# Performance work log

Hardware: AMD Instinct MI355X
Metric: run time of the kernel (lower is better)

The kernel has to match this reference:

```python
import jax, jax.numpy as jnp
import numpy as np

N_HEAD = 16
N_EMBD = 1024

def setup_inputs() -> dict:
    key = jax.random.key(0)
    ks = jax.random.split(key, 7)
    B, S, D = 2, 2048, N_EMBD
    scale = 1.0 / np.sqrt(D)
    return {
        "x": jax.random.normal(ks[0], (B, S, D), dtype=jnp.float32),
        "Wq": jax.random.normal(ks[1], (D, D), dtype=jnp.float32) * scale,
        "bq": jnp.zeros((D,), dtype=jnp.float32),
        "Wk": jax.random.normal(ks[2], (D, D), dtype=jnp.float32) * scale,
        "bk": jnp.zeros((D,), dtype=jnp.float32),
        "Wv": jax.random.normal(ks[3], (D, D), dtype=jnp.float32) * scale,
        "bv": jnp.zeros((D,), dtype=jnp.float32),
    }

def reference(x, Wq, bq, Wk, bk, Wv, bv):
    B, S, D = x.shape
    H = N_HEAD
    hd = D // H
    # QKV projections
    q = (x @ Wq + bq).reshape(B, S, H, hd).transpose(0, 2, 1, 3)  # [B,H,S,hd]
    k = (x @ Wk + bk).reshape(B, S, H, hd).transpose(0, 2, 1, 3)
    v = (x @ Wv + bv).reshape(B, S, H, hd).transpose(0, 2, 1, 3)
    # Note: original module defines a causal mask but never applies it.
    att = jnp.einsum("bhqd,bhkd->bhqk", q, k) * (1.0 / jnp.sqrt(hd).astype(x.dtype))
    att = jax.nn.softmax(att, axis=-1)
    y = jnp.einsum("bhqk,bhkd->bhqd", att, v)  # [B,H,S,hd]
    return y.transpose(0, 2, 1, 3).reshape(B, S, D)
```

## Files before the change

### kernel.cpp

```cpp
#include <hip/hip_runtime.h>


#define D_MODEL 1024
#define NHEAD   16
#define HDIM    64
#define SEQ     2048
#define MROWS   4096
#define CSC     0.18033688011112042f

typedef __attribute__((ext_vector_type(8))) short short8;
typedef __attribute__((ext_vector_type(4))) float f32x4;

__device__ __forceinline__ float bf2f(unsigned short u) {
  return __uint_as_float(((unsigned int)u) << 16);
}
__device__ __forceinline__ unsigned short f2bf(float f) {
  unsigned int u = __float_as_uint(f);
  u += 0x7fff + ((u >> 16) & 1);
  return (unsigned short)(u >> 16);
}
__device__ __forceinline__ unsigned int cvtpk_bf16(float lo, float hi) {
  unsigned int r;
  asm("v_cvt_pk_bf16_f32 %0, %1, %2" : "=v"(r) : "v"(lo), "v"(hi));
  return r;
}

__device__ __forceinline__ int sniff_bf16(const unsigned short* x) {
  int cnt = 0;
#pragma unroll
  for (int i = 0; i < 64; ++i) {
    const unsigned e = (x[2 * i] >> 7) & 0xFF;
    cnt += (e >= 105 && e <= 140) ? 1 : 0;
  }
  return cnt >= 48;
}

__device__ __forceinline__ void gl_lds16(const unsigned short* g, unsigned short* l) {
  __builtin_amdgcn_global_load_lds(
      (const __attribute__((address_space(1))) unsigned int*)g,
      (__attribute__((address_space(3))) unsigned int*)l, 16, 0, 0);
}

__global__ __launch_bounds__(256) void cvt_x(const unsigned short* __restrict__ X,
                                             unsigned short* __restrict__ Xbf) {
  const int isbf = sniff_bf16(X);
  const size_t i0 = ((size_t)blockIdx.x * 256 + threadIdx.x) * 8;
  if (isbf) {
    *(uint4*)(Xbf + i0) = *(const uint4*)(X + i0);
  } else {
    const float* Xf = (const float*)X;
    const float4 f0 = *(const float4*)(Xf + i0);
    const float4 f1 = *(const float4*)(Xf + i0 + 4);
    unsigned int t[4] = {cvtpk_bf16(f0.x, f0.y), cvtpk_bf16(f0.z, f0.w),
                         cvtpk_bf16(f1.x, f1.y), cvtpk_bf16(f1.z, f1.w)};
    *(uint4*)(Xbf + i0) = *(const uint4*)t;
  }
}

__global__ __launch_bounds__(256) void cvt_w(
    const unsigned short* __restrict__ w0, const unsigned short* __restrict__ w1,
    const unsigned short* __restrict__ w2,
    const unsigned short* __restrict__ b0, const unsigned short* __restrict__ b1,
    const unsigned short* __restrict__ b2,
    unsigned short* __restrict__ Wt, unsigned short* __restrict__ bb) {
  __shared__ unsigned short tile[32][33];
  const int z = blockIdx.z;
  const unsigned short* W    = (z == 0) ? w0 : ((z == 1) ? w1 : w2);
  const unsigned short* bias = (z == 0) ? b0 : ((z == 1) ? b1 : b2);
  unsigned short* Wtz = Wt + ((size_t)z << 20);
  const int isbf = sniff_bf16(W);
  const int bx = blockIdx.x * 32;
  const int by = blockIdx.y * 32;
  const int tx = threadIdx.x & 31;
  const int ty = threadIdx.x >> 5;
#pragma unroll
  for (int r = ty; r < 32; r += 8) {
    unsigned short v;
    if (isbf) v = W[(size_t)(by + r) * D_MODEL + bx + tx];
    else      v = f2bf(((const float*)W)[(size_t)(by + r) * D_MODEL + bx + tx]);
    tile[r][tx] = v;
  }
  __syncthreads();
#pragma unroll
  for (int r = ty; r < 32; r += 8)
    Wtz[(size_t)(bx + r) * D_MODEL + by + tx] = tile[tx][r];
  if (blockIdx.x == 0 && blockIdx.y == 0) {
    const int i0 = threadIdx.x * 4;
#pragma unroll
    for (int j = 0; j < 4; ++j)
      bb[z * D_MODEL + i0 + j] =
          isbf ? bias[i0 + j] : f2bf(((const float*)bias)[i0 + j]);
  }
}

__device__ __forceinline__ void store_cd(int z, unsigned short* Out, int row0,
                                         int col, const f32x4 acc, float bb,
                                         float sc) {
  if (z == 2) {
    const int b = row0 >> 11, s = row0 & 2047;
    const int bh = b * NHEAD + (col >> 6);
    uint2 pk;
    pk.x = cvtpk_bf16(acc[0] + bb, acc[1] + bb);
    pk.y = cvtpk_bf16(acc[2] + bb, acc[3] + bb);
    *(uint2*)(Out + ((size_t)bh * HDIM + (col & 63)) * SEQ + s) = pk;
  } else {
#pragma unroll
    for (int r = 0; r < 4; ++r)
      Out[(size_t)(row0 + r) * D_MODEL + col] = f2bf((acc[r] + bb) * sc);
  }
}

__global__ __launch_bounds__(256) void qkv_gemm_fast(
    const unsigned short* __restrict__ Xbf, const unsigned short* __restrict__ Wt,
    const unsigned short* __restrict__ bb,
    unsigned short* __restrict__ Oq, unsigned short* __restrict__ Ok,
    unsigned short* __restrict__ Ov) {
  const int z = blockIdx.z;
  const unsigned short* Wz = Wt + ((size_t)z << 20);
  unsigned short* Out = (z == 0) ? Oq : ((z == 1) ? Ok : Ov);
  const float sc = (z == 0) ? CSC : 1.0f;

  __shared__ unsigned short As[128 * 32];
  __shared__ unsigned short Bs[128 * 32];

  const int tid  = threadIdx.x;
  const int wave = tid >> 6, lane = tid & 63;
  const int wm = wave >> 1, wn = wave & 1;
  const int lrow = lane & 15, lk = lane >> 4;
  const int m0 = blockIdx.y * 128;
  const int n0 = blockIdx.x * 128;

  f32x4 acc[4][4] = {};

  for (int kk = 0; kk < D_MODEL; kk += 32) {
#pragma unroll
    for (int i = 0; i < 2; ++i) {
      const int c = i * 256 + tid;
      const int row = c >> 2, off = (c & 3) * 8;
      gl_lds16(Xbf + (size_t)(m0 + row) * D_MODEL + kk + off, &As[c * 8]);
      gl_lds16(Wz  + (size_t)(n0 + row) * D_MODEL + kk + off, &Bs[c * 8]);
    }
    __syncthreads();
    short8 a[4], b[4];
#pragma unroll
    for (int t = 0; t < 4; ++t) {
      a[t] = *(const short8*)(&As[(wm * 64 + t * 16 + lrow) * 32 + lk * 8]);
      b[t] = *(const short8*)(&Bs[(wn * 64 + t * 16 + lrow) * 32 + lk * 8]);
    }
#pragma unroll
    for (int mt = 0; mt < 4; ++mt)
#pragma unroll
      for (int nt = 0; nt < 4; ++nt)
        acc[mt][nt] = __builtin_amdgcn_mfma_f32_16x16x32_bf16(a[mt], b[nt], acc[mt][nt], 0, 0, 0);
    __syncthreads();
  }
#pragma unroll
  for (int nt = 0; nt < 4; ++nt) {
    const int col = n0 + wn * 64 + nt * 16 + lrow;
    const float bv = bf2f(bb[z * D_MODEL + col]);
#pragma unroll
    for (int mt = 0; mt < 4; ++mt)
      store_cd(z, Out, m0 + wm * 64 + mt * 16 + lk * 4, col, acc[mt][nt], bv, sc);
  }
}

#define LDA 40
__global__ __launch_bounds__(256) void qkv_gemm_med(
    const unsigned short* __restrict__ X, const unsigned short* __restrict__ Wt,
    const unsigned short* __restrict__ bb,
    unsigned short* __restrict__ Oq, unsigned short* __restrict__ Ok,
    unsigned short* __restrict__ Ov) {
  const int z = blockIdx.z;
  const unsigned short* Wz = Wt + ((size_t)z << 20);
  unsigned short* Out = (z == 0) ? Oq : ((z == 1) ? Ok : Ov);
  const float sc = (z == 0) ? CSC : 1.0f;

  __shared__ alignas(16) unsigned short As[128 * LDA];
  __shared__ alignas(16) unsigned short Bs[128 * LDA];

  const int isbf = sniff_bf16(X);
  const int tid  = threadIdx.x;
  const int wave = tid >> 6, lane = tid & 63;
  const int wm = wave >> 1, wn = wave & 1;
  const int lrow = lane & 15, lk = lane >> 4;
  const int m0 = blockIdx.y * 128;
  const int n0 = blockIdx.x * 128;

  f32x4 acc[4][4] = {};

  for (int kk = 0; kk < D_MODEL; kk += 32) {
#pragma unroll
    for (int i = 0; i < 2; ++i) {
      const int c = tid + i * 256;
      const int row = c >> 2, off = (c & 3) * 8;
      if (isbf) {
        *(uint4*)(&As[row * LDA + off]) =
            *(const uint4*)(X + (size_t)(m0 + row) * D_MODEL + kk + off);
      } else {
        const float* Xf = (const float*)X;
        const float4 f0 = *(const float4*)(Xf + (size_t)(m0 + row) * D_MODEL + kk + off);
        const float4 f1 = *(const float4*)(Xf + (size_t)(m0 + row) * D_MODEL + kk + off + 4);
        unsigned int t[4] = {cvtpk_bf16(f0.x, f0.y), cvtpk_bf16(f0.z, f0.w),
                             cvtpk_bf16(f1.x, f1.y), cvtpk_bf16(f1.z, f1.w)};
        *(uint4*)(&As[row * LDA + off]) = *(const uint4*)t;
      }
      *(uint4*)(&Bs[row * LDA + off]) =
          *(const uint4*)(Wz + (size_t)(n0 + row) * D_MODEL + kk + off);
    }
    __syncthreads();
    short8 a[4], b[4];
#pragma unroll
    for (int t = 0; t < 4; ++t) {
      a[t] = *(const short8*)(&As[(wm * 64 + t * 16 + lrow) * LDA + lk * 8]);
      b[t] = *(const short8*)(&Bs[(wn * 64 + t * 16 + lrow) * LDA + lk * 8]);
    }
#pragma unroll
    for (int mt = 0; mt < 4; ++mt)
#pragma unroll
      for (int nt = 0; nt < 4; ++nt)
        acc[mt][nt] = __builtin_amdgcn_mfma_f32_16x16x32_bf16(a[mt], b[nt], acc[mt][nt], 0, 0, 0);
    __syncthreads();
  }
#pragma unroll
  for (int nt = 0; nt < 4; ++nt) {
    const int col = n0 + wn * 64 + nt * 16 + lrow;
    const float bv = bf2f(bb[z * D_MODEL + col]);
#pragma unroll
    for (int mt = 0; mt < 4; ++mt)
      store_cd(z, Out, m0 + wm * 64 + mt * 16 + lk * 4, col, acc[mt][nt], bv, sc);
  }
}

__global__ __launch_bounds__(256) void qkv_gemm(
    const unsigned short* __restrict__ X,
    const unsigned short* __restrict__ Wq, const unsigned short* __restrict__ Wk,
    const unsigned short* __restrict__ Wv,
    const unsigned short* __restrict__ bq, const unsigned short* __restrict__ bk,
    const unsigned short* __restrict__ bv,
    unsigned short* __restrict__ Oq, unsigned short* __restrict__ Ok,
    unsigned short* __restrict__ Ov) {
  const int z = blockIdx.z;
  const unsigned short* W    = (z == 0) ? Wq : ((z == 1) ? Wk : Wv);
  const unsigned short* bias = (z == 0) ? bq : ((z == 1) ? bk : bv);
  unsigned short*       Out  = (z == 0) ? Oq : ((z == 1) ? Ok : Ov);
  const float sc = (z == 0) ? CSC : 1.0f;

  __shared__ alignas(16) unsigned short As[128 * LDA];
  __shared__ alignas(16) unsigned short Bs[128 * LDA];

  const int isbf = sniff_bf16(X);
  const int tid  = threadIdx.x;
  const int wave = tid >> 6, lane = tid & 63;
  const int wm = wave >> 1, wn = wave & 1;
  const int lrow = lane & 15, lk = lane >> 4;
  const int m0 = blockIdx.y * 128;
  const int n0 = blockIdx.x * 128;

  f32x4 acc[4][4] = {};

  for (int kk = 0; kk < D_MODEL; kk += 32) {
#pragma unroll
    for (int i = 0; i < 2; ++i) {
      const int c = tid + i * 256;
      const int row = c >> 2, off = (c & 3) * 8;
      if (isbf) {
        *(uint4*)(&As[row * LDA + off]) =
            *(const uint4*)(X + (size_t)(m0 + row) * D_MODEL + kk + off);
      } else {
        const float* Xf = (const float*)X;
        const float4 f0 = *(const float4*)(Xf + (size_t)(m0 + row) * D_MODEL + kk + off);
        const float4 f1 = *(const float4*)(Xf + (size_t)(m0 + row) * D_MODEL + kk + off + 4);
        unsigned int t[4] = {cvtpk_bf16(f0.x, f0.y), cvtpk_bf16(f0.z, f0.w),
                             cvtpk_bf16(f1.x, f1.y), cvtpk_bf16(f1.z, f1.w)};
        *(uint4*)(&As[row * LDA + off]) = *(const uint4*)t;
      }
    }
#pragma unroll
    for (int i = 0; i < 2; ++i) {
      const int c = tid + i * 256;
      const int krow = c & 31;
      const int nc0 = (c >> 5) * 8;
      if (isbf) {
        uint4 v = *(const uint4*)(W + (size_t)(kk + krow) * D_MODEL + n0 + nc0);
        const unsigned short* e = (const unsigned short*)&v;
#pragma unroll
        for (int j = 0; j < 8; ++j) Bs[(nc0 + j) * LDA + krow] = e[j];
      } else {
        const float* Wf = (const float*)W;
        const float4 f0 = *(const float4*)(Wf + (size_t)(kk + krow) * D_MODEL + n0 + nc0);
        const float4 f1 = *(const float4*)(Wf + (size_t)(kk + krow) * D_MODEL + n0 + nc0 + 4);
        const float vals[8] = {f0.x, f0.y, f0.z, f0.w, f1.x, f1.y, f1.z, f1.w};
#pragma unroll
        for (int j = 0; j < 8; ++j) Bs[(nc0 + j) * LDA + krow] = f2bf(vals[j]);
      }
    }
    __syncthreads();
    short8 a[4], b[4];
#pragma unroll
    for (int t = 0; t < 4; ++t) {
      a[t] = *(const short8*)(&As[(wm * 64 + t * 16 + lrow) * LDA + lk * 8]);
      b[t] = *(const short8*)(&Bs[(wn * 64 + t * 16 + lrow) * LDA + lk * 8]);
    }
#pragma unroll
    for (int mt = 0; mt < 4; ++mt)
#pragma unroll
      for (int nt = 0; nt < 4; ++nt)
        acc[mt][nt] = __builtin_amdgcn_mfma_f32_16x16x32_bf16(a[mt], b[nt], acc[mt][nt], 0, 0, 0);
    __syncthreads();
  }
#pragma unroll
  for (int nt = 0; nt < 4; ++nt) {
    const int col = n0 + wn * 64 + nt * 16 + lrow;
    const float bv2 = isbf ? bf2f(bias[col]) : ((const float*)bias)[col];
#pragma unroll
    for (int mt = 0; mt < 4; ++mt)
      store_cd(z, Out, m0 + wm * 64 + mt * 16 + lk * 4, col, acc[mt][nt], bv2, sc);
  }
}

__device__ __forceinline__ int swz(int row, int colu) {
  return row * 64 + (colu ^ ((row & 7) << 3));
}
__global__ __launch_bounds__(256, 4) void attn(
    const unsigned short* __restrict__ Qg, const unsigned short* __restrict__ Kg,
    const unsigned short* __restrict__ Vtg, unsigned short* __restrict__ Outg,
    const unsigned short* __restrict__ Xs) {
  const int lin = blockIdx.y * 32 + blockIdx.x;
  const int xcd = lin & 7, idx = lin >> 3;
  const int bh = xcd * 4 + (idx >> 5);
  const int qt = idx & 31;
  const int b = bh >> 4, h = bh & 15;
  const size_t baseR = (size_t)b * SEQ * D_MODEL + h * HDIM;
  const size_t baseV = (size_t)bh * HDIM * SEQ;

  __shared__ alignas(16) unsigned short Ks[64 * 64];
  __shared__ alignas(16) unsigned short Vs[64 * 64];
  __shared__ alignas(16) unsigned short Ps[64 * 64];

  const int isbf = sniff_bf16(Xs);
  const int tid  = threadIdx.x;
  const int wave = tid >> 6, lane = tid & 63;
  const int lrow = lane & 15, lk = lane >> 4;
  const int q0 = qt * 64;
  const int wq = wave * 16;

  const int c0 = tid,       r0 = c0 >> 3, g0 = ((c0 & 7) ^ (r0 & 7)) * 8;
  const int c1 = tid + 256, r1 = c1 >> 3, g1 = ((c1 & 7) ^ (r1 & 7)) * 8;
  const unsigned short* Kg0 = Kg  + baseR + (size_t)r0 * D_MODEL + g0;
  const unsigned short* Kg1 = Kg  + baseR + (size_t)r1 * D_MODEL + g1;
  const unsigned short* Vg0 = Vtg + baseV + (size_t)r0 * SEQ + g0;
  const unsigned short* Vg1 = Vtg + baseV + (size_t)r1 * SEQ + g1;

  short8 qf[2];
#pragma unroll
  for (int ks = 0; ks < 2; ++ks)
    qf[ks] = *(const short8*)(Qg + baseR +
        (size_t)(q0 + wq + lrow) * D_MODEL + ks * 32 + lk * 8);

  f32x4 accO[4] = {};
  float lsum = 0.f;

#pragma unroll 1
  for (int kv0 = 0; kv0 < SEQ; kv0 += 64) {
    __syncthreads();
    gl_lds16(Kg0 + (size_t)kv0 * D_MODEL, &Ks[c0 * 8]);
    gl_lds16(Kg1 + (size_t)kv0 * D_MODEL, &Ks[c1 * 8]);
    gl_lds16(Vg0 + kv0, &Vs[c0 * 8]);
    gl_lds16(Vg1 + kv0, &Vs[c1 * 8]);
    __syncthreads();

    f32x4 accST[4] = {};
#pragma unroll
    for (int ks = 0; ks < 2; ++ks) {
      short8 kf[4];
#pragma unroll
      for (int mt = 0; mt < 4; ++mt)
        kf[mt] = *(const short8*)(&Ks[swz(mt * 16 + lrow, ks * 32 + lk * 8)]);
#pragma unroll
      for (int mt = 0; mt < 4; ++mt)
        accST[mt] = __builtin_amdgcn_mfma_f32_16x16x32_bf16(
            kf[mt], qf[ks], accST[mt], 0, 0, 0);
    }

#pragma unroll
    for (int mt = 0; mt < 4; ++mt) {
      const float p0 = exp2f(accST[mt][0]), p1 = exp2f(accST[mt][1]);
      const float p2 = exp2f(accST[mt][2]), p3 = exp2f(accST[mt][3]);
      lsum += (p0 + p1) + (p2 + p3);
      uint2 pk;
      pk.x = cvtpk_bf16(p0, p1);
      pk.y = cvtpk_bf16(p2, p3);
      *(uint2*)(&Ps[swz(wq + lrow, mt * 16 + lk * 4)]) = pk;
    }

#pragma unroll
    for (int ks = 0; ks < 2; ++ks) {
      short8 vf[4];
      const short8 pf = *(const short8*)(&Ps[swz(wq + lrow, ks * 32 + lk * 8)]);
#pragma unroll
      for (int nd = 0; nd < 4; ++nd)
        vf[nd] = *(const short8*)(&Vs[swz(nd * 16 + lrow, ks * 32 + lk * 8)]);
#pragma unroll
      for (int nd = 0; nd < 4; ++nd)
        accO[nd] = __builtin_amdgcn_mfma_f32_16x16x32_bf16(
            pf, vf[nd], accO[nd], 0, 0, 0);
    }
  }

  lsum += __shfl_xor(lsum, 16, 64);
  lsum += __shfl_xor(lsum, 32, 64);
  __syncthreads();
  float* Lf = (float*)Ps;
  if (lk == 0) Lf[wq + lrow] = lsum;
  __syncthreads();
  const f32x4 l4 = *(const f32x4*)(&Lf[wq + lk * 4]);
#pragma unroll
  for (int r = 0; r < 4; ++r) {
    const float inv = 1.0f / l4[r];
    const int row = q0 + wq + lk * 4 + r;
#pragma unroll
    for (int nd = 0; nd < 4; ++nd) {
      const int col = h * HDIM + nd * 16 + lrow;
      const float val = accO[nd][r] * inv;
      const size_t idx = (size_t)b * SEQ * D_MODEL + (size_t)row * D_MODEL + col;
      if (isbf) Outg[idx] = f2bf(val);
      else      ((float*)Outg)[idx] = val;
    }
  }
}

extern "C" void kernel_launch(void* const* d_in, const int* in_sizes, int n_in,
                              void* d_out, int out_size, void* d_ws, size_t ws_size,
                              hipStream_t stream) {
  const unsigned short* x  = (const unsigned short*)d_in[0];
  const unsigned short* Wq = (const unsigned short*)d_in[1];
  const unsigned short* bq = (const unsigned short*)d_in[2];
  const unsigned short* Wk = (const unsigned short*)d_in[3];
  const unsigned short* bk = (const unsigned short*)d_in[4];
  const unsigned short* Wv = (const unsigned short*)d_in[5];
  const unsigned short* bv = (const unsigned short*)d_in[6];
  unsigned short* out = (unsigned short*)d_out;
  unsigned short* ws  = (unsigned short*)d_ws;

  const size_t M1 = 1u << 20;
  const size_t wsE = ws_size / 2;

  unsigned short* Wt  = ws;
  unsigned short* bb  = ws + 3 * M1;
  unsigned short* K   = ws + 3 * M1 + 65536;
  unsigned short* Vt  = K + 4 * M1;
  unsigned short* Xbf = Vt + 4 * M1;
  unsigned short* Q;

  if (wsE >= 19 * M1 + 65536) {
    Q = Xbf + 4 * M1;
    cvt_x<<<dim3(2048), 256, 0, stream>>>(x, Xbf);
    cvt_w<<<dim3(32, 32, 3), 256, 0, stream>>>(Wq, Wk, Wv, bq, bk, bv, Wt, bb);
    qkv_gemm_fast<<<dim3(8, 32, 3), 256, 0, stream>>>(Xbf, Wt, bb, Q, K, Vt);
  } else if (wsE >= 15 * M1 + 65536) {
    Q = out;
    cvt_x<<<dim3(2048), 256, 0, stream>>>(x, Xbf);
    cvt_w<<<dim3(32, 32, 3), 256, 0, stream>>>(Wq, Wk, Wv, bq, bk, bv, Wt, bb);
    qkv_gemm_fast<<<dim3(8, 32, 3), 256, 0, stream>>>(Xbf, Wt, bb, Q, K, Vt);
  } else if (wsE >= 11 * M1 + 65536) {
    Q = out;
    cvt_w<<<dim3(32, 32, 3), 256, 0, stream>>>(Wq, Wk, Wv, bq, bk, bv, Wt, bb);
    qkv_gemm_med<<<dim3(8, 32, 3), 256, 0, stream>>>(x, Wt, bb, Q, K, Vt);
  } else {
    if (wsE >= 12 * M1) { Q = ws; K = ws + 4 * M1; Vt = ws + 8 * M1; }
    else                { Q = out; K = ws; Vt = ws + 4 * M1; }
    qkv_gemm<<<dim3(8, 32, 3), 256, 0, stream>>>(x, Wq, Wk, Wv, bq, bk, bv, Q, K, Vt);
  }
  attn<<<dim3(32, 32), 256, 0, stream>>>(Q, K, Vt, out, x);
}
```

Baseline: 192.2 us.

## Double-buffer K/V tiles in attention and raise MFMA wave priority

Splits the K and V shared-memory tiles into A/B buffers so the next tile's global-to-LDS loads are issued before computing on the current tile. This removes one of the two barriers per iteration and overlaps load latency with MFMA and exp work. It also wraps the MFMA sections in s_setprio to favor matrix-issue waves. LDS use grows from 24KB to 40KB per block, which may reduce occupancy below the 4 blocks per CU requested.

```diff
diff --git a/kernel.cpp b/kernel.cpp
--- a/kernel.cpp
+++ b/kernel.cpp
@@ -321,6 +321,56 @@
 __device__ __forceinline__ int swz(int row, int colu) {
   return row * 64 + (colu ^ ((row & 7) << 3));
 }
+
+#define ATTN_PHASE(KSC, VSC, KSN, VSN, NXT)                                    \
+  {                                                                            \
+    if ((NXT) < SEQ) {               \
+      gl_lds16(Kg0 + (size_t)(NXT) * D_MODEL, &(KSN)[c0 * 8]);                 \
+      gl_lds16(Kg1 + (size_t)(NXT) * D_MODEL, &(KSN)[c1 * 8]);                 \
+      gl_lds16(Vg0 + (NXT), &(VSN)[c0 * 8]);                                   \
+      gl_lds16(Vg1 + (NXT), &(VSN)[c1 * 8]);                                   \
+    }                                                                          \
+    f32x4 accST[4] = {};                                                       \
+    __builtin_amdgcn_s_setprio(1);                                             \
+    _Pragma("unroll")                                                          \
+    for (int ks = 0; ks < 2; ++ks) {                                           \
+      short8 kf[4];                                                            \
+      _Pragma("unroll")                                                        \
+      for (int mt = 0; mt < 4; ++mt)                                           \
+        kf[mt] = *(const short8*)(&(KSC)[swz(mt * 16 + lrow, ks * 32 + lk * 8)]); \
+      _Pragma("unroll")                                                        \
+      for (int mt = 0; mt < 4; ++mt)                                           \
+        accST[mt] = __builtin_amdgcn_mfma_f32_16x16x32_bf16(                   \
+            kf[mt], qf[ks], accST[mt], 0, 0, 0);                               \
+    }                                                                          \
+    __builtin_amdgcn_s_setprio(0);                                             \
+    _Pragma("unroll")                                                          \
+    for (int mt = 0; mt < 4; ++mt) {                                           \
+      const float p0 = exp2f(accST[mt][0]), p1 = exp2f(accST[mt][1]);          \
+      const float p2 = exp2f(accST[mt][2]), p3 = exp2f(accST[mt][3]);          \
+      lsum += (p0 + p1) + (p2 + p3);                                           \
+      uint2 pk;                                                                \
+      pk.x = cvtpk_bf16(p0, p1);                                               \
+      pk.y = cvtpk_bf16(p2, p3);                                               \
+      *(uint2*)(&Ps[swz(wq + lrow, mt * 16 + lk * 4)]) = pk;                   \
+    }                                                                          \
+    __builtin_amdgcn_s_setprio(1);                                             \
+    _Pragma("unroll")                                                          \
+    for (int ks = 0; ks < 2; ++ks) {                                           \
+      short8 vf[4];                                                            \
+      const short8 pf = *(const short8*)(&Ps[swz(wq + lrow, ks * 32 + lk * 8)]); \
+      _Pragma("unroll")                                                        \
+      for (int nd = 0; nd < 4; ++nd)                                           \
+        vf[nd] = *(const short8*)(&(VSC)[swz(nd * 16 + lrow, ks * 32 + lk * 8)]); \
+      _Pragma("unroll")                                                        \
+      for (int nd = 0; nd < 4; ++nd)                                           \
+        accO[nd] = __builtin_amdgcn_mfma_f32_16x16x32_bf16(                    \
+            pf, vf[nd], accO[nd], 0, 0, 0);                                    \
+    }                                                                          \
+    __builtin_amdgcn_s_setprio(0);                                             \
+    __syncthreads();    \
+  }
+
 __global__ __launch_bounds__(256, 4) void attn(
     const unsigned short* __restrict__ Qg, const unsigned short* __restrict__ Kg,
     const unsigned short* __restrict__ Vtg, unsigned short* __restrict__ Outg,
@@ -333,8 +383,10 @@
   const size_t baseR = (size_t)b * SEQ * D_MODEL + h * HDIM;
   const size_t baseV = (size_t)bh * HDIM * SEQ;
 
-  __shared__ alignas(16) unsigned short Ks[64 * 64];
-  __shared__ alignas(16) unsigned short Vs[64 * 64];
+  __shared__ alignas(16) unsigned short KsA[64 * 64];
+  __shared__ alignas(16) unsigned short KsB[64 * 64];
+  __shared__ alignas(16) unsigned short VsA[64 * 64];
+  __shared__ alignas(16) unsigned short VsB[64 * 64];
   __shared__ alignas(16) unsigned short Ps[64 * 64];
 
   const int isbf = sniff_bf16(Xs);
@@ -360,51 +412,16 @@
   f32x4 accO[4] = {};
   float lsum = 0.f;
 
+  gl_lds16(Kg0, &KsA[c0 * 8]);
+  gl_lds16(Kg1, &KsA[c1 * 8]);
+  gl_lds16(Vg0, &VsA[c0 * 8]);
+  gl_lds16(Vg1, &VsA[c1 * 8]);
+  __syncthreads();
+
 #pragma unroll 1
-  for (int kv0 = 0; kv0 < SEQ; kv0 += 64) {
-    __syncthreads();
-    gl_lds16(Kg0 + (size_t)kv0 * D_MODEL, &Ks[c0 * 8]);
-    gl_lds16(Kg1 + (size_t)kv0 * D_MODEL, &Ks[c1 * 8]);
-    gl_lds16(Vg0 + kv0, &Vs[c0 * 8]);
-    gl_lds16(Vg1 + kv0, &Vs[c1 * 8]);
-    __syncthreads();
-
-    f32x4 accST[4] = {};
-#pragma unroll
-    for (int ks = 0; ks < 2; ++ks) {
-      short8 kf[4];
-#pragma unroll
-      for (int mt = 0; mt < 4; ++mt)
-        kf[mt] = *(const short8*)(&Ks[swz(mt * 16 + lrow, ks * 32 + lk * 8)]);
-#pragma unroll
-      for (int mt = 0; mt < 4; ++mt)
-        accST[mt] = __builtin_amdgcn_mfma_f32_16x16x32_bf16(
-            kf[mt], qf[ks], accST[mt], 0, 0, 0);
-    }
-
-#pragma unroll
-    for (int mt = 0; mt < 4; ++mt) {
-      const float p0 = exp2f(accST[mt][0]), p1 = exp2f(accST[mt][1]);
-      const float p2 = exp2f(accST[mt][2]), p3 = exp2f(accST[mt][3]);
-      lsum += (p0 + p1) + (p2 + p3);
-      uint2 pk;
-      pk.x = cvtpk_bf16(p0, p1);
-      pk.y = cvtpk_bf16(p2, p3);
-      *(uint2*)(&Ps[swz(wq + lrow, mt * 16 + lk * 4)]) = pk;
-    }
-
-#pragma unroll
-    for (int ks = 0; ks < 2; ++ks) {
-      short8 vf[4];
-      const short8 pf = *(const short8*)(&Ps[swz(wq + lrow, ks * 32 + lk * 8)]);
-#pragma unroll
-      for (int nd = 0; nd < 4; ++nd)
-        vf[nd] = *(const short8*)(&Vs[swz(nd * 16 + lrow, ks * 32 + lk * 8)]);
-#pragma unroll
-      for (int nd = 0; nd < 4; ++nd)
-        accO[nd] = __builtin_amdgcn_mfma_f32_16x16x32_bf16(
-            pf, vf[nd], accO[nd], 0, 0, 0);
-    }
+  for (int kv0 = 0; kv0 < SEQ; kv0 += 128) {
+    ATTN_PHASE(KsA, VsA, KsB, VsB, kv0 + 64);
+    ATTN_PHASE(KsB, VsB, KsA, VsA, kv0 + 128);
   }
 
   lsum += __shfl_xor(lsum, 16, 64);
```

New measurement: 193.2 us. No clear change (+0.5%).
